# Optimization experiments

Measured on AMD Instinct MI355X. Metric: run time of the kernel, lower is better.

The kernel has to match this reference:

```python
import jax, jax.numpy as jnp
import numpy as np

N_IMG, BATCH, SEQ, D_IN, H = 32, 1024, 64, 16, 16


def setup_inputs() -> dict:
    key = jax.random.key(0)
    k1, k2, k3, k4, k5 = jax.random.split(key, 5)
    s = 1.0 / np.sqrt(H)  # torch nn.LSTM default init: U(-1/sqrt(H), 1/sqrt(H))
    return {
        "images": jax.random.normal(k1, (N_IMG, BATCH, SEQ, D_IN), jnp.float32),
        "w_ih": jax.random.uniform(k2, (4 * H, D_IN), jnp.float32, -s, s),
        "w_hh": jax.random.uniform(k3, (4 * H, H), jnp.float32, -s, s),
        "b_ih": jax.random.uniform(k4, (4 * H,), jnp.float32, -s, s),
        "b_hh": jax.random.uniform(k5, (4 * H,), jnp.float32, -s, s),
    }


def reference(images, w_ih, w_hh, b_ih, b_hh):
    # images: [N, B, S, D]. The torch module loops over N chunks, feeding each
    # [B, S, D] chunk through nn.LSTM while carrying (h, c) across chunks.
    # Equivalent: one continuous recurrence over N*S timesteps.
    n, b, s, d = images.shape
    h_dim = w_hh.shape[1]
    # time-major: [N*S, B, D]
    xs = images.transpose(0, 2, 1, 3).reshape(n * s, b, d)
    # precompute input projections for all timesteps (the only big GEMM)
    x_proj = jnp.einsum('tbd,gd->tbg', xs, w_ih) + (b_ih + b_hh)  # [T, B, 4H]

    def cell(carry, xp_t):
        h_prev, c_prev = carry
        gates = xp_t + h_prev @ w_hh.T  # [B, 4H]; torch gate order: i, f, g, o
        i, f, g, o = jnp.split(gates, 4, axis=-1)
        c = jax.nn.sigmoid(f) * c_prev + jax.nn.sigmoid(i) * jnp.tanh(g)
        h_new = jax.nn.sigmoid(o) * jnp.tanh(c)
        return (h_new, c), h_new

    h0 = jnp.zeros((b, h_dim), images.dtype)
    (_, _), outs = jax.lax.scan(cell, (h0, h0), x_proj)  # outs: [T, B, H]
    # torch stacks per-chunk outputs [B, S, H] along dim 0 -> [N, B, S, H]
    return outs.reshape(n, s, b, h_dim).transpose(0, 2, 1, 3)
```

## Files before the change

### kernel.cpp

```cpp
#include <hip/hip_runtime.h>

#define LOG2E      1.44269504088896340736f
#define TWO_LOG2E  2.88539008177792680472f

typedef float f16v __attribute__((ext_vector_type(16)));

__device__ __forceinline__ float frcp(float x)  { return __builtin_amdgcn_rcpf(x); }
__device__ __forceinline__ float fexp2(float x) { return __builtin_amdgcn_exp2f(x); }

__device__ __forceinline__ void gload_lds16(const float* g, float* l) {
    auto gp = (const __attribute__((address_space(1))) float*)g;
    auto lp = (__attribute__((address_space(3))) float*)l;
    __builtin_amdgcn_global_load_lds(gp, lp, 16, 0, 0);
}


__global__ __launch_bounds__(256, 1)
void lstm_fused(const float* __restrict__ images,
                const float* __restrict__ w_ih,
                const float* __restrict__ w_hh,
                const float* __restrict__ b_ih,
                const float* __restrict__ b_hh,
                float* __restrict__ out)
{
    __shared__ float4 warm[4][256];

    const int lane = threadIdx.x & 63;
    const int wid  = threadIdx.x >> 6;
    const int b    = (blockIdx.x << 2) + wid;
    const int a    = lane >> 4;
    const int j    = lane & 15;

    asm volatile("" :: "v"(&warm[wid][0]) : "memory");

    int rr1 = __builtin_amdgcn_update_dpp(0, j, 0x121, 0xF, 0xF, true);
    const int d_ror = (rr1 - j) & 15;

    int e16;
    { int pa = a, pb = a;
      asm volatile("s_nop 1\n\t"
                   "v_permlane16_swap_b32 %0, %1" : "+v"(pa), "+v"(pb));
      e16 = pa & 1; }
    int e32;
    { int pc = a, pd = a;
      asm volatile("s_nop 1\n\t"
                   "v_permlane32_swap_b32 %0, %1" : "+v"(pc), "+v"(pd));
      e32 = (pc < 2) ? 0 : 1; }

    const int m1 = ((a >> 1) == e32);
    const int m0 = ((a & 1) == e16);
    const int gate = m0 ? (m1 ? 1 : 2) : (m1 ? 0 : 3);
    const int r = gate * 16 + j;

    const float aa = (gate == 2) ? TWO_LOG2E : -LOG2E;
    const float mm = (gate == 2) ? -2.0f * TWO_LOG2E : 1.0f;
    const float dd = (gate == 2) ? TWO_LOG2E : 0.0f;

    float whh[16];
#pragma unroll
    for (int t = 0; t < 16; ++t)
        whh[t] = aa * w_hh[r * 16 + ((j + d_ror * t) & 15)];
    float wih[16];
#pragma unroll
    for (int k = 0; k < 16; ++k)
        wih[k] = aa * w_ih[r * 16 + k];
    const float bias = aa * (b_ih[r] + b_hh[r]);

    const bool su0 = (a == 0), su1 = (a == 1), su2 = (a == 2), su3 = (a == 3);

    float hv = 0.0f;
    float c  = 0.0f;
    float sv = 0.0f;

    const int bbase = b << 10;
    const unsigned wb = __builtin_amdgcn_readfirstlane(b);
    const unsigned long long img_u = (unsigned long long)images;

#define PB(p) ((((p) >> 4) << 20) + bbase + (((((p) << 2)) & 63) << 4))

#define SBASE(p) (img_u + (((unsigned long long)((p) >> 4)) << 22)             \
                        + (((unsigned long long)wb) << 12)                     \
                        + (unsigned long long)(((p) & 15) << 8))

#define WARM_CHUNK(n) {                                                        \
        const float* gp_ = images + ((n) << 20) + bbase + (lane << 2);         \
        float4* lb_ = &warm[wid][0];                                           \
        gload_lds16(gp_ + 0,   (float*)(lb_ + 0));                             \
        gload_lds16(gp_ + 256, (float*)(lb_ + 64));                            \
        gload_lds16(gp_ + 512, (float*)(lb_ + 128));                           \
        gload_lds16(gp_ + 768, (float*)(lb_ + 192)); }

#define SLOADP(Qraw) {                                                         \
        int Q_ = (Qraw); if (Q_ > 511) Q_ = 511;                               \
        unsigned long long sb_ = SBASE(Q_);                                    \
        asm volatile("s_load_dwordx16 %0, %4, 0x0\n\t"                         \
                     "s_load_dwordx16 %1, %4, 0x40\n\t"                        \
                     "s_load_dwordx16 %2, %4, 0x80\n\t"                        \
                     "s_load_dwordx16 %3, %4, 0xc0"                            \
                     : "=s"(sx0), "=s"(sx1), "=s"(sx2), "=s"(sx3)              \
                     : "s"(sb_));                                              \
    }

#define WAIT_LGKM() { asm volatile("s_waitcnt lgkmcnt(0)" ::: "memory");       \
                      __builtin_amdgcn_sched_barrier(0); }

#define PROJ1(dst, sx) {                                                       \
        float s0_ = bias, s1_ = 0.f, s2_ = 0.f, s3_ = 0.f;                     \
        _Pragma("unroll")                                                      \
        for (int k_ = 0; k_ < 4; ++k_) {                                       \
            s0_ = fmaf(sx[4*k_+0], wih[4*k_+0], s0_);                          \
            s1_ = fmaf(sx[4*k_+1], wih[4*k_+1], s1_);                          \
            s2_ = fmaf(sx[4*k_+2], wih[4*k_+2], s2_);                          \
            s3_ = fmaf(sx[4*k_+3], wih[4*k_+3], s3_);                          \
        }                                                                      \
        dst = (s0_ + s1_) + (s2_ + s3_);                                       \
    }
#define PROJ4() { PROJ1(xpre[0], sx0); PROJ1(xpre[1], sx1);                    \
                  PROJ1(xpre[2], sx2); PROJ1(xpre[3], sx3); }

#define STEP(SU, xpv) {                                                        \
        float p0 = (xpv), p1, p2, p3;                                          \
        asm("s_nop 1\n\t"                                                      \
          "v_fmac_f32 %[q0], %[h], %[w0]\n\t"                                  \
          "v_mul_f32 %[q1], %[h], %[w1] row_ror:1 row_mask:0xf bank_mask:0xf\n\t" \
          "v_mul_f32 %[q2], %[h], %[w2] row_ror:2 row_mask:0xf bank_mask:0xf\n\t" \
          "v_mul_f32 %[q3], %[h], %[w3] row_ror:3 row_mask:0xf bank_mask:0xf\n\t" \
          "v_fmac_f32 %[q0], %[h], %[w4] row_ror:4 row_mask:0xf bank_mask:0xf\n\t" \
          "v_fmac_f32 %[q1], %[h], %[w5] row_ror:5 row_mask:0xf bank_mask:0xf\n\t" \
          "v_fmac_f32 %[q2], %[h], %[w6] row_ror:6 row_mask:0xf bank_mask:0xf\n\t" \
          "v_fmac_f32 %[q3], %[h], %[w7] row_ror:7 row_mask:0xf bank_mask:0xf\n\t" \
          "v_fmac_f32 %[q0], %[h], %[w8] row_ror:8 row_mask:0xf bank_mask:0xf\n\t" \
          "v_fmac_f32 %[q1], %[h], %[w9] row_ror:9 row_mask:0xf bank_mask:0xf\n\t" \
          "v_fmac_f32 %[q2], %[h], %[w10] row_ror:10 row_mask:0xf bank_mask:0xf\n\t" \
          "v_fmac_f32 %[q3], %[h], %[w11] row_ror:11 row_mask:0xf bank_mask:0xf\n\t" \
          "v_fmac_f32 %[q0], %[h], %[w12] row_ror:12 row_mask:0xf bank_mask:0xf\n\t" \
          "v_fmac_f32 %[q1], %[h], %[w13] row_ror:13 row_mask:0xf bank_mask:0xf\n\t" \
          "v_fmac_f32 %[q2], %[h], %[w14] row_ror:14 row_mask:0xf bank_mask:0xf\n\t" \
          "v_fmac_f32 %[q3], %[h], %[w15] row_ror:15 row_mask:0xf bank_mask:0xf"   \
          : [q0]"+v"(p0), [q1]"=&v"(p1), [q2]"=&v"(p2), [q3]"=&v"(p3)          \
          : [h]"v"(hv),                                                        \
            [w0]"v"(whh[0]),  [w1]"v"(whh[1]),  [w2]"v"(whh[2]),  [w3]"v"(whh[3]), \
            [w4]"v"(whh[4]),  [w5]"v"(whh[5]),  [w6]"v"(whh[6]),  [w7]"v"(whh[7]), \
            [w8]"v"(whh[8]),  [w9]"v"(whh[9]),  [w10]"v"(whh[10]),[w11]"v"(whh[11]),\
            [w12]"v"(whh[12]),[w13]"v"(whh[13]),[w14]"v"(whh[14]),[w15]"v"(whh[15]));\
        float arg = (p0 + p1) + (p2 + p3);                                     \
        float act = fmaf(mm, frcp(1.0f + fexp2(arg)), dd);                     \
        float qf, qg, qi, qo;                                                  \
        asm("v_mov_b32 %[A], %[x]\n\t"                                         \
          "v_mov_b32 %[B], %[x]\n\t"                                           \
          "s_nop 1\n\t"                                                        \
          "v_permlane16_swap_b32 %[A], %[B]\n\t"                               \
          "v_mov_b32 %[C], %[A]\n\t"                                           \
          "v_mov_b32 %[D], %[B]\n\t"                                           \
          "v_permlane32_swap_b32 %[A], %[C]\n\t"                               \
          "v_permlane32_swap_b32 %[B], %[D]"                                   \
          : [A]"=&v"(qf), [B]"=&v"(qi), [C]"=&v"(qg), [D]"=&v"(qo)             \
          : [x]"v"(act));                                                      \
        float ig = qi * qg;                                                    \
        float qo2 = qo + qo;                                                   \
        c = fmaf(c, qf, ig);                                                   \
        float rr = frcp(1.0f + fexp2(c));                                      \
        hv = fmaf(-qo2, rr, qo);                                               \
        sv = (SU) ? hv : sv;                                                   \
    }

#define STORE(pb) out[(pb) + lane] = sv;

    f16v  sx0, sx1, sx2, sx3;
    float xpre[4];

    WARM_CHUNK(0);
    WARM_CHUNK(1);
    SLOADP(0);
    WAIT_LGKM();
    PROJ4();

#pragma unroll 1
    for (int P = 0; P < 512; ++P) {
        SLOADP(P + 1);
        {
            const int pb = PB(P);
            STEP(su0, xpre[0]);
            STEP(su1, xpre[1]);
            STEP(su2, xpre[2]);
            STEP(su3, xpre[3]);
            STORE(pb);
        }
        if ((P & 15) == 14 && P < 480)
            WARM_CHUNK((P >> 4) + 2);
        WAIT_LGKM();
        PROJ4();
    }

#undef STEP
#undef STORE
#undef PROJ4
#undef PROJ1
#undef WAIT_LGKM
#undef SLOADP
#undef WARM_CHUNK
#undef SBASE
#undef PB
}

extern "C" void kernel_launch(void* const* d_in, const int* in_sizes, int n_in,
                              void* d_out, int out_size, void* d_ws, size_t ws_size,
                              hipStream_t stream)
{
    const float* images = (const float*)d_in[0];
    const float* w_ih   = (const float*)d_in[1];
    const float* w_hh   = (const float*)d_in[2];
    const float* b_ih   = (const float*)d_in[3];
    const float* b_hh   = (const float*)d_in[4];
    float* outp         = (float*)d_out;

    lstm_fused<<<dim3(256), dim3(256), 0, stream>>>(images, w_ih, w_hh, b_ih, b_hh, outp);
}
```

Baseline: 316.3 us.

## Interleave two batch recurrences per wave to hide serial latency

Each wave now carries two independent batch elements (A and B) and alternates their LSTM steps, so one chain's DPP, transcendental and permlane latency can overlap the other's. The grid is halved to 128 blocks and the scalar loads fetch half-period chunks for both elements, with the wait split into two places per iteration. This halves the number of active waves, using fewer CUs, in exchange for more instruction-level parallelism inside each wave.

Result: slower. 600.0 us (+89.7%).

```diff
diff --git a/kernel.cpp b/kernel.cpp
--- a/kernel.cpp
+++ b/kernel.cpp
@@ -4,6 +4,7 @@
 #define TWO_LOG2E  2.88539008177792680472f
 
 typedef float f16v __attribute__((ext_vector_type(16)));
+typedef unsigned long long ull;
 
 __device__ __forceinline__ float frcp(float x)  { return __builtin_amdgcn_rcpf(x); }
 __device__ __forceinline__ float fexp2(float x) { return __builtin_amdgcn_exp2f(x); }
@@ -27,7 +28,8 @@
 
     const int lane = threadIdx.x & 63;
     const int wid  = threadIdx.x >> 6;
-    const int b    = (blockIdx.x << 2) + wid;
+    const int w    = (blockIdx.x << 2) + wid;
+    const int b0   = w << 1;
     const int a    = lane >> 4;
     const int j    = lane & 15;
 
@@ -68,36 +70,37 @@
 
     const bool su0 = (a == 0), su1 = (a == 1), su2 = (a == 2), su3 = (a == 3);
 
-    float hv = 0.0f;
-    float c  = 0.0f;
-    float sv = 0.0f;
-
-    const int bbase = b << 10;
-    const unsigned wb = __builtin_amdgcn_readfirstlane(b);
-    const unsigned long long img_u = (unsigned long long)images;
-
-#define PB(p) ((((p) >> 4) << 20) + bbase + (((((p) << 2)) & 63) << 4))
-
-#define SBASE(p) (img_u + (((unsigned long long)((p) >> 4)) << 22)             \
-                        + (((unsigned long long)wb) << 12)                     \
-                        + (unsigned long long)(((p) & 15) << 8))
+    float hvA = 0.0f, cA = 0.0f, svA = 0.0f;
+    float hvB = 0.0f, cB = 0.0f, svB = 0.0f;
+
+    const int bbA = b0 << 10;
+    const int bbB = bbA + 1024;
+    const unsigned wb = __builtin_amdgcn_readfirstlane(b0);
+    const ull img_u = (ull)images;
+
+#define PBC(p, bb) ((((p) >> 4) << 20) + (bb) + (((((p) << 2)) & 63) << 4))
 
 #define WARM_CHUNK(n) {                                                        \
-        const float* gp_ = images + ((n) << 20) + bbase + (lane << 2);         \
+        const float* gp_ = images + ((n) << 20) + bbA + (lane << 2);           \
         float4* lb_ = &warm[wid][0];                                           \
-        gload_lds16(gp_ + 0,   (float*)(lb_ + 0));                             \
-        gload_lds16(gp_ + 256, (float*)(lb_ + 64));                            \
-        gload_lds16(gp_ + 512, (float*)(lb_ + 128));                           \
-        gload_lds16(gp_ + 768, (float*)(lb_ + 192)); }
-
-#define SLOADP(Qraw) {                                                         \
-        int Q_ = (Qraw); if (Q_ > 511) Q_ = 511;                               \
-        unsigned long long sb_ = SBASE(Q_);                                    \
+        gload_lds16(gp_ + 0,    (float*)(lb_ + 0));                            \
+        gload_lds16(gp_ + 256,  (float*)(lb_ + 64));                           \
+        gload_lds16(gp_ + 512,  (float*)(lb_ + 128));                          \
+        gload_lds16(gp_ + 768,  (float*)(lb_ + 192));                          \
+        gload_lds16(gp_ + 1024, (float*)(lb_ + 0));                            \
+        gload_lds16(gp_ + 1280, (float*)(lb_ + 64));                           \
+        gload_lds16(gp_ + 1536, (float*)(lb_ + 128));                          \
+        gload_lds16(gp_ + 1792, (float*)(lb_ + 192)); }
+
+#define SLOAD2(HPraw) {                                                        \
+        int hp_ = (HPraw); if (hp_ > 1023) hp_ = 1023;                         \
+        ull sb_ = img_u + ((ull)(hp_ >> 5) << 22) + ((ull)wb << 12)            \
+                        + (ull)((hp_ & 31) << 7);                              \
         asm volatile("s_load_dwordx16 %0, %4, 0x0\n\t"                         \
                      "s_load_dwordx16 %1, %4, 0x40\n\t"                        \
-                     "s_load_dwordx16 %2, %4, 0x80\n\t"                        \
-                     "s_load_dwordx16 %3, %4, 0xc0"                            \
-                     : "=s"(sx0), "=s"(sx1), "=s"(sx2), "=s"(sx3)              \
+                     "s_load_dwordx16 %2, %4, 0x1000\n\t"                      \
+                     "s_load_dwordx16 %3, %4, 0x1040"                          \
+                     : "=s"(sxA0), "=s"(sxA1), "=s"(sxB0), "=s"(sxB1)          \
                      : "s"(sb_));                                              \
     }
 
@@ -115,10 +118,8 @@
         }                                                                      \
         dst = (s0_ + s1_) + (s2_ + s3_);                                       \
     }
-#define PROJ4() { PROJ1(xpre[0], sx0); PROJ1(xpre[1], sx1);                    \
-                  PROJ1(xpre[2], sx2); PROJ1(xpre[3], sx3); }
-
-#define STEP(SU, xpv) {                                                        \
+
+#define STEP(HV, CC, SV, SU, xpv) {                                            \
         float p0 = (xpv), p1, p2, p3;                                          \
         asm("s_nop 1\n\t"                                                      \
           "v_fmac_f32 %[q0], %[h], %[w0]\n\t"                                  \
@@ -138,7 +139,7 @@
           "v_fmac_f32 %[q2], %[h], %[w14] row_ror:14 row_mask:0xf bank_mask:0xf\n\t" \
           "v_fmac_f32 %[q3], %[h], %[w15] row_ror:15 row_mask:0xf bank_mask:0xf"   \
           : [q0]"+v"(p0), [q1]"=&v"(p1), [q2]"=&v"(p2), [q3]"=&v"(p3)          \
-          : [h]"v"(hv),                                                        \
+          : [h]"v"(HV),                                                        \
             [w0]"v"(whh[0]),  [w1]"v"(whh[1]),  [w2]"v"(whh[2]),  [w3]"v"(whh[3]), \
             [w4]"v"(whh[4]),  [w5]"v"(whh[5]),  [w6]"v"(whh[6]),  [w7]"v"(whh[7]), \
             [w8]"v"(whh[8]),  [w9]"v"(whh[9]),  [w10]"v"(whh[10]),[w11]"v"(whh[11]),\
@@ -158,49 +159,53 @@
           : [x]"v"(act));                                                      \
         float ig = qi * qg;                                                    \
         float qo2 = qo + qo;                                                   \
-        c = fmaf(c, qf, ig);                                                   \
-        float rr = frcp(1.0f + fexp2(c));                                      \
-        hv = fmaf(-qo2, rr, qo);                                               \
-        sv = (SU) ? hv : sv;                                                   \
-    }
-
-#define STORE(pb) out[(pb) + lane] = sv;
-
-    f16v  sx0, sx1, sx2, sx3;
-    float xpre[4];
+        CC = fmaf(CC, qf, ig);                                                 \
+        float rr = frcp(1.0f + fexp2(CC));                                     \
+        HV = fmaf(-qo2, rr, qo);                                               \
+        SV = (SU) ? HV : SV;                                                   \
+    }
+
+    f16v  sxA0, sxA1, sxB0, sxB1;
+    float xpA[4], xpB[4];
 
     WARM_CHUNK(0);
     WARM_CHUNK(1);
-    SLOADP(0);
+    SLOAD2(0);
     WAIT_LGKM();
-    PROJ4();
+    PROJ1(xpA[0], sxA0); PROJ1(xpA[1], sxA1);
+    PROJ1(xpB[0], sxB0); PROJ1(xpB[1], sxB1);
+    SLOAD2(1);
 
 #pragma unroll 1
     for (int P = 0; P < 512; ++P) {
-        SLOADP(P + 1);
-        {
-            const int pb = PB(P);
-            STEP(su0, xpre[0]);
-            STEP(su1, xpre[1]);
-            STEP(su2, xpre[2]);
-            STEP(su3, xpre[3]);
-            STORE(pb);
-        }
+        STEP(hvA, cA, svA, su0, xpA[0]);
+        STEP(hvB, cB, svB, su0, xpB[0]);
+        STEP(hvA, cA, svA, su1, xpA[1]);
+        STEP(hvB, cB, svB, su1, xpB[1]);
+        WAIT_LGKM();
+        PROJ1(xpA[2], sxA0); PROJ1(xpA[3], sxA1);
+        PROJ1(xpB[2], sxB0); PROJ1(xpB[3], sxB1);
+        SLOAD2(2 * P + 2);
+        STEP(hvA, cA, svA, su2, xpA[2]);
+        STEP(hvB, cB, svB, su2, xpB[2]);
+        STEP(hvA, cA, svA, su3, xpA[3]);
+        STEP(hvB, cB, svB, su3, xpB[3]);
+        out[PBC(P, bbA) + lane] = svA;
+        out[PBC(P, bbB) + lane] = svB;
         if ((P & 15) == 14 && P < 480)
             WARM_CHUNK((P >> 4) + 2);
         WAIT_LGKM();
-        PROJ4();
+        PROJ1(xpA[0], sxA0); PROJ1(xpA[1], sxA1);
+        PROJ1(xpB[0], sxB0); PROJ1(xpB[1], sxB1);
+        SLOAD2(2 * P + 3);
     }
 
 #undef STEP
-#undef STORE
-#undef PROJ4
 #undef PROJ1
 #undef WAIT_LGKM
-#undef SLOADP
+#undef SLOAD2
 #undef WARM_CHUNK
-#undef SBASE
-#undef PB
+#undef PBC
 }
 
 extern "C" void kernel_launch(void* const* d_in, const int* in_sizes, int n_in,
@@ -214,5 +219,5 @@
     const float* b_hh   = (const float*)d_in[4];
     float* outp         = (float*)d_out;
 
-    lstm_fused<<<dim3(256), dim3(256), 0, stream>>>(images, w_ih, w_hh, b_ih, b_hh, outp);
+    lstm_fused<<<dim3(128), dim3(256), 0, stream>>>(images, w_ih, w_hh, b_ih, b_hh, outp);
 }
```
